# Kernel optimization log

Measured on AMD Instinct MI355X. Metric: run time of the kernel, lower is better.

Reference implementation:

```python
import jax, jax.numpy as jnp
import numpy as np

NUM_HEADS = 4   # num_heads init kwarg
KERNEL = 7      # kernel_size init kwarg
EPS = 1e-5      # nn.LayerNorm default eps


def setup_inputs() -> dict:
    key = jax.random.key(0)
    ks = jax.random.split(key, 6)
    C, depth = 128, 2
    x = jax.random.normal(ks[0], (2, C, 64, 64), jnp.float32)
    qkv_w = jax.random.normal(ks[1], (depth, 3 * C, C), jnp.float32) * 0.05
    qkv_b = jnp.zeros((depth, 3 * C), jnp.float32)
    rpb = jax.random.normal(ks[2], (depth, NUM_HEADS, 2 * KERNEL - 1, 2 * KERNEL - 1), jnp.float32) * 0.02
    proj_w = jax.random.normal(ks[3], (depth, C, C), jnp.float32) * 0.05
    proj_b = jnp.zeros((depth, C), jnp.float32)
    ln_g = jnp.ones((C,), jnp.float32)
    ln_b = jnp.zeros((C,), jnp.float32)
    return dict(x=x, qkv_w=qkv_w, qkv_b=qkv_b, rpb=rpb,
                proj_w=proj_w, proj_b=proj_b, ln_g=ln_g, ln_b=ln_b)


def _na2d(x, w_qkv, b_qkv, rpb, w_p, b_p):
    """NATTEN-style 2D neighborhood attention. x: (B,H,W,C)."""
    B, H, W, C = x.shape
    h, k = NUM_HEADS, KERNEL
    d = C // h
    qkv = (x @ w_qkv.T + b_qkv).reshape(B, H, W, 3, h, d)
    q = qkv[..., 0, :, :] * (d ** -0.5)   # (B,H,W,h,d)
    kk = qkv[..., 1, :, :]
    v = qkv[..., 2, :, :]
    # edge-clamped window starts: each query sees exactly k x k neighbors
    si = jnp.clip(jnp.arange(H) - k // 2, 0, H - k)
    sj = jnp.clip(jnp.arange(W) - k // 2, 0, W - k)
    idx_i = si[:, None] + jnp.arange(k)   # (H,k) absolute row indices
    idx_j = sj[:, None] + jnp.arange(k)   # (W,k) absolute col indices

    def win(t):  # (B,H,W,h,d) -> (B,H,W,k,k,h,d)
        t = t[:, idx_i]          # (B,H,k,W,h,d)
        t = t[:, :, :, idx_j]    # (B,H,k,W,k,h,d)
        return jnp.transpose(t, (0, 1, 3, 2, 4, 5, 6))

    kw = win(kk)
    vw = win(v)
    attn = jnp.einsum('bijhd,bijpqhd->bijhpq', q, kw)  # (B,H,W,h,k,k)
    # relative position bias: index = (neighbor_abs - query) + (k-1)
    bi = jnp.arange(k)[None, :] + (k - 1) - (jnp.arange(H) - si)[:, None]  # (H,k)
    bj = jnp.arange(k)[None, :] + (k - 1) - (jnp.arange(W) - sj)[:, None]  # (W,k)
    bias = rpb[:, bi[:, None, :, None], bj[None, :, None, :]]  # (h,H,W,k,k)
    attn = attn + jnp.transpose(bias, (1, 2, 0, 3, 4))[None]
    attn = jax.nn.softmax(attn.reshape(B, H, W, h, k * k), axis=-1).reshape(B, H, W, h, k, k)
    out = jnp.einsum('bijhpq,bijpqhd->bijhd', attn, vw).reshape(B, H, W, C)
    return out @ w_p.T + b_p


def reference(x, qkv_w, qkv_b, rpb, proj_w, proj_b, ln_g, ln_b):
    y = jnp.transpose(x, (0, 2, 3, 1))  # NCHW -> NHWC
    for l in range(qkv_w.shape[0]):     # depth=2 stacked NA layers
        y = _na2d(y, qkv_w[l], qkv_b[l], rpb[l], proj_w[l], proj_b[l])
    mu = y.mean(-1, keepdims=True)
    var = y.var(-1, keepdims=True)
    y = (y - mu) / jnp.sqrt(var + EPS) * ln_g + ln_b
    return jnp.transpose(y, (0, 3, 1, 2))  # NHWC -> NCHW
```

## Files before the change

### kernel.cpp

```cpp
#include <hip/hip_runtime.h>
#include <hip/hip_bf16.h>
#include <math.h>

#define PIX 8192
typedef __hip_bfloat16 bf16;
typedef __attribute__((ext_vector_type(8))) short short8;
typedef __attribute__((ext_vector_type(4))) float f32x4;

__device__ inline float bflo(unsigned u) { return __uint_as_float(u << 16); }
__device__ inline float bfhi(unsigned u) { return __uint_as_float(u & 0xffff0000u); }
__device__ inline unsigned short f2b(float f) {
  __hip_bfloat16 h = __float2bfloat16(f);
  return *reinterpret_cast<unsigned short*>(&h);
}
__device__ inline unsigned pack2(float a, float b) {
  return (unsigned)f2b(a) | ((unsigned)f2b(b) << 16);
}

__global__ __launch_bounds__(256) void prep(const float* __restrict__ x,
                                            const float* __restrict__ qw,
                                            const float* __restrict__ pw,
                                            unsigned short* __restrict__ y,
                                            unsigned short* __restrict__ wq,
                                            unsigned short* __restrict__ wp) {
  int tid = threadIdx.x;
  if (blockIdx.x >= 128) {
    int idx = (blockIdx.x - 128) * 256 + tid;
    if (idx < 98304) wq[idx] = f2b(qw[idx]);
    if (idx < 32768) wp[idx] = f2b(pw[idx]);
    return;
  }
  __shared__ float tile[64][129];
  int blk = blockIdx.x;
  int b = blk >> 6, i = blk & 63;
  const float* xbase = x + (size_t)b * 128 * 4096 + (size_t)i * 64;
  for (int idx = tid; idx < 8192; idx += 256) {
    int c = idx >> 6, j = idx & 63;
    tile[j][c] = xbase[(size_t)c * 4096 + j];
  }
  __syncthreads();
  unsigned short* yrow = y + (size_t)blk * 64 * 128;
  for (int idx = tid; idx < 8192; idx += 256) {
    int j = idx >> 7, c = idx & 127;
    yrow[idx] = f2b(tile[j][c]);
  }
}

__global__ __launch_bounds__(256) void gemm_mfma(const unsigned short* __restrict__ A,
                                                 const unsigned short* __restrict__ W,
                                                 const float* __restrict__ bias,
                                                 unsigned short* __restrict__ Cmat,
                                                 int N) {
  int m0 = blockIdx.x * 64, n0 = blockIdx.y * 64;
  int tid = threadIdx.x;
  int w = tid >> 6, lane = tid & 63;
  int quad = lane >> 4, l16 = lane & 15;

  const short8* ap =
      (const short8*)(A + (size_t)(m0 + w * 16 + l16) * 128 + quad * 8);
  short8 a[4];
#pragma unroll
  for (int kc = 0; kc < 4; ++kc) a[kc] = ap[kc * 4];

  f32x4 acc[4];
#pragma unroll
  for (int nt = 0; nt < 4; ++nt) {
    const short8* bp =
        (const short8*)(W + (size_t)(n0 + nt * 16 + l16) * 128 + quad * 8);
    f32x4 c = {0.f, 0.f, 0.f, 0.f};
#pragma unroll
    for (int kc = 0; kc < 4; ++kc)
      c = __builtin_amdgcn_mfma_f32_16x16x32_bf16(a[kc], bp[kc * 4], c, 0, 0, 0);
    acc[nt] = c;
  }

#pragma unroll
  for (int nt = 0; nt < 4; ++nt) {
    int col = n0 + nt * 16 + l16;
    float bv = bias[col];
#pragma unroll
    for (int r = 0; r < 4; ++r) {
      int m = m0 + w * 16 + quad * 4 + r;
      Cmat[(size_t)m * N + col] = f2b(acc[nt][r] + bv);
    }
  }
}

#define RSTRIDE 72
__global__ __launch_bounds__(256, 2) void na_attn(const unsigned short* __restrict__ qkvp,
                                                  const float* __restrict__ rpb,
                                                  unsigned short* __restrict__ out) {
  __shared__ __align__(16) unsigned short kbuf[140 * RSTRIDE];
  __shared__ __align__(16) unsigned short vbuf[140 * RSTRIDE];
  __shared__ float rb[338];
  __shared__ float sc[64][52];

  int ti = blockIdx.x >> 4, tj = blockIdx.x & 15;
  int hp = blockIdx.y;
  int bz = blockIdx.z;
  int tid = threadIdx.x;
  int bi0 = ti * 8 - 3, bj0 = tj * 4 - 3;

  for (int t = tid; t < 338; t += 256) rb[t] = rpb[hp * 338 + t];

  for (int t = tid; t < 2240; t += 256) {
    int row = t >> 4;
    int sub = t & 15;
    int isv = sub >> 3;
    int c = sub & 7;
    int ri = row / 10, rj = row - ri * 10;
    int gi = bi0 + ri, gj = bj0 + rj;
    uint4 val = make_uint4(0, 0, 0, 0);
    if ((unsigned)gi < 64u && (unsigned)gj < 64u) {
      int pixn = (bz * 64 + gi) * 64 + gj;
      val = *(const uint4*)(qkvp + (size_t)pixn * 384 + 128 + isv * 128 +
                            hp * 64 + c * 8);
    }
    *(uint4*)((isv ? vbuf : kbuf) + row * RSTRIDE + c * 8) = val;
  }
  __syncthreads();

  int r = tid & 3;
  int hl = (tid >> 2) & 1;
  int px = tid >> 3;
  int ph = px * 2 + hl;
  int pi = px >> 2, pj = px & 3;
  int i = ti * 8 + pi, j = tj * 4 + pj;
  int si = min(max(i - 3, 0), 57), sj = min(max(j - 3, 0), 57);
  int li = si - bi0, lj = sj - bj0;
  int oi = i - si, oj = j - sj;
  int H = hp * 2 + hl;
  int pix = (bz * 64 + i) * 64 + j;

  const float scale = 0.17677669529663687f;
  float q[8];
  {
    uint4 t = *(const uint4*)(qkvp + (size_t)pix * 384 + H * 32 + r * 8);
    q[0] = bflo(t.x) * scale;  q[1] = bfhi(t.x) * scale;
    q[2] = bflo(t.y) * scale;  q[3] = bfhi(t.y) * scale;
    q[4] = bflo(t.z) * scale;  q[5] = bfhi(t.z) * scale;
    q[6] = bflo(t.w) * scale;  q[7] = bfhi(t.w) * scale;
  }

  const unsigned short* kh = kbuf + hl * 32 + r * 8;
  const unsigned short* vh = vbuf + hl * 32 + r * 8;
  const float* rbh = rb + hl * 169;

#pragma unroll
  for (int p = 0; p < 7; ++p) {
#pragma unroll
    for (int qq = 0; qq < 7; ++qq) {
      int n = (li + p) * 10 + (lj + qq);
      uint4 t = *(const uint4*)(kh + n * RSTRIDE);
      float dot = q[0] * bflo(t.x) + q[1] * bfhi(t.x)
                + q[2] * bflo(t.y) + q[3] * bfhi(t.y)
                + q[4] * bflo(t.z) + q[5] * bfhi(t.z)
                + q[6] * bflo(t.w) + q[7] * bfhi(t.w);
      dot += __shfl_xor(dot, 1);
      dot += __shfl_xor(dot, 2);
      if (r == 0) sc[ph][p * 7 + qq] = dot + rbh[(p + 6 - oi) * 13 + (qq + 6 - oj)];
    }
  }
  __syncthreads();

  float m = -INFINITY;
#pragma unroll
  for (int n = 0; n < 49; ++n) m = fmaxf(m, sc[ph][n]);

  float sum = 0.f;
  float acc[8] = {0.f, 0.f, 0.f, 0.f, 0.f, 0.f, 0.f, 0.f};
#pragma unroll
  for (int p = 0; p < 7; ++p) {
#pragma unroll
    for (int qq = 0; qq < 7; ++qq) {
      float e = __expf(sc[ph][p * 7 + qq] - m);
      sum += e;
      int n = (li + p) * 10 + (lj + qq);
      uint4 t = *(const uint4*)(vh + n * RSTRIDE);
      acc[0] += e * bflo(t.x);  acc[1] += e * bfhi(t.x);
      acc[2] += e * bflo(t.y);  acc[3] += e * bfhi(t.y);
      acc[4] += e * bflo(t.z);  acc[5] += e * bfhi(t.z);
      acc[6] += e * bflo(t.w);  acc[7] += e * bfhi(t.w);
    }
  }
  float inv = 1.f / sum;
  uint4 t;
  t.x = pack2(acc[0] * inv, acc[1] * inv);
  t.y = pack2(acc[2] * inv, acc[3] * inv);
  t.z = pack2(acc[4] * inv, acc[5] * inv);
  t.w = pack2(acc[6] * inv, acc[7] * inv);
  *(uint4*)(out + (size_t)pix * 128 + H * 32 + r * 8) = t;
}

__global__ __launch_bounds__(256) void ln_out(const unsigned short* __restrict__ y,
                                              const float* __restrict__ g,
                                              const float* __restrict__ bta,
                                              float* __restrict__ out) {
  __shared__ float tile[64][129];
  __shared__ float mean_s[64], rstd_s[64];
  int blk = blockIdx.x;
  int b = blk >> 6, i = blk & 63;
  int tid = threadIdx.x;
  const unsigned short* yrow = y + (size_t)blk * 64 * 128;
  for (int idx = tid; idx < 8192; idx += 256) {
    int j = idx >> 7, c = idx & 127;
    tile[j][c] = __uint_as_float((unsigned)yrow[idx] << 16);
  }
  __syncthreads();
  int jj = tid >> 2, qtr = tid & 3;
  float sum = 0.f, sumsq = 0.f;
#pragma unroll
  for (int cc = 0; cc < 32; ++cc) {
    float v = tile[jj][qtr * 32 + cc];
    sum += v; sumsq += v * v;
  }
  sum += __shfl_xor(sum, 1);  sum += __shfl_xor(sum, 2);
  sumsq += __shfl_xor(sumsq, 1);  sumsq += __shfl_xor(sumsq, 2);
  if (qtr == 0) {
    float mu = sum * (1.f / 128.f);
    mean_s[jj] = mu;
    rstd_s[jj] = rsqrtf(sumsq * (1.f / 128.f) - mu * mu + 1e-5f);
  }
  __syncthreads();
  int c0 = tid >> 6;
  int j = tid & 63;
  for (int c = c0; c < 128; c += 4) {
    float v = (tile[j][c] - mean_s[j]) * rstd_s[j] * g[c] + bta[c];
    out[(((size_t)b * 128 + c) * 64 + i) * 64 + j] = v;
  }
}

extern "C" void kernel_launch(void* const* d_in, const int* in_sizes, int n_in,
                              void* d_out, int out_size, void* d_ws, size_t ws_size,
                              hipStream_t stream) {
  (void)in_sizes; (void)n_in; (void)out_size; (void)ws_size;
  const float* x   = (const float*)d_in[0];
  const float* qw  = (const float*)d_in[1];
  const float* qb  = (const float*)d_in[2];
  const float* rpb = (const float*)d_in[3];
  const float* pw  = (const float*)d_in[4];
  const float* pb  = (const float*)d_in[5];
  const float* lg  = (const float*)d_in[6];
  const float* lb  = (const float*)d_in[7];

  unsigned short* y    = (unsigned short*)d_ws;
  unsigned short* qkv  = y + (size_t)PIX * 128;
  unsigned short* wq   = qkv + (size_t)PIX * 384;
  unsigned short* wp   = wq + 98304;
  unsigned short* attn = (unsigned short*)d_out;
  float* out = (float*)d_out;

  prep<<<512, 256, 0, stream>>>(x, qw, pw, y, wq, wp);
  for (int l = 0; l < 2; ++l) {
    gemm_mfma<<<dim3(128, 6), 256, 0, stream>>>(y, wq + l * 49152, qb + l * 384, qkv, 384);
    na_attn<<<dim3(128, 2, 2), 256, 0, stream>>>(qkv, rpb + l * 676, attn);
    gemm_mfma<<<dim3(128, 2), 256, 0, stream>>>(attn, wp + l * 16384, pb + l * 128, y, 128);
  }
  ln_out<<<128, 256, 0, stream>>>(y, lg, lb, out);
}
```

Measured before the change: 146.6 us.

## Fuse layer-0 projection with layer-1 QKV GEMM and final projection with LayerNorm

Replaces the per-layer launch loop with a fixed sequence in which the layer-0 output projection and the layer-1 QKV projection run in one kernel, with the intermediate activations kept in shared memory. The final output projection is fused into the LayerNorm/transpose kernel. This removes two kernel launches and the global round-trip of the projected activations. In exchange, the fused kernels use only 128 blocks, which gives less parallelism than the separate GEMM grids. They also read weights directly from global memory without tiling.

Result: no change. 148.7 us (+1.4%).

```diff
diff --git a/kernel.cpp b/kernel.cpp
--- a/kernel.cpp
+++ b/kernel.cpp
@@ -192,21 +192,102 @@
   *(uint4*)(out + (size_t)pix * 128 + H * 32 + r * 8) = t;
 }
 
-__global__ __launch_bounds__(256) void ln_out(const unsigned short* __restrict__ y,
-                                              const float* __restrict__ g,
-                                              const float* __restrict__ bta,
-                                              float* __restrict__ out) {
+#define PSTRIDE 136
+__global__ __launch_bounds__(256) void projqkv(const unsigned short* __restrict__ attnp,
+                                               const unsigned short* __restrict__ wp0,
+                                               const float* __restrict__ pb0,
+                                               const unsigned short* __restrict__ wq1,
+                                               const float* __restrict__ qb1,
+                                               unsigned short* __restrict__ qkvout) {
+  __shared__ __align__(16) unsigned short po[64 * PSTRIDE];
+  int m0 = blockIdx.x * 64;
+  int tid = threadIdx.x;
+  int w = tid >> 6, lane = tid & 63;
+  int quad = lane >> 4, l16 = lane & 15;
+
+  {
+    const short8* ap =
+        (const short8*)(attnp + (size_t)(m0 + w * 16 + l16) * 128 + quad * 8);
+    short8 a[4];
+#pragma unroll
+    for (int kc = 0; kc < 4; ++kc) a[kc] = ap[kc * 4];
+#pragma unroll
+    for (int nt = 0; nt < 8; ++nt) {
+      const short8* bp =
+          (const short8*)(wp0 + (size_t)(nt * 16 + l16) * 128 + quad * 8);
+      f32x4 c = {0.f, 0.f, 0.f, 0.f};
+#pragma unroll
+      for (int kc = 0; kc < 4; ++kc)
+        c = __builtin_amdgcn_mfma_f32_16x16x32_bf16(a[kc], bp[kc * 4], c, 0, 0, 0);
+      float bv = pb0[nt * 16 + l16];
+#pragma unroll
+      for (int r2 = 0; r2 < 4; ++r2)
+        po[(w * 16 + quad * 4 + r2) * PSTRIDE + nt * 16 + l16] = f2b(c[r2] + bv);
+    }
+  }
+  __syncthreads();
+
+  {
+    short8 a[4];
+#pragma unroll
+    for (int kc = 0; kc < 4; ++kc)
+      a[kc] = *(const short8*)(po + (w * 16 + l16) * PSTRIDE + kc * 32 + quad * 8);
+#pragma unroll
+    for (int nt = 0; nt < 24; ++nt) {
+      const short8* bp =
+          (const short8*)(wq1 + (size_t)(nt * 16 + l16) * 128 + quad * 8);
+      f32x4 c = {0.f, 0.f, 0.f, 0.f};
+#pragma unroll
+      for (int kc = 0; kc < 4; ++kc)
+        c = __builtin_amdgcn_mfma_f32_16x16x32_bf16(a[kc], bp[kc * 4], c, 0, 0, 0);
+      int col = nt * 16 + l16;
+      float bv = qb1[col];
+#pragma unroll
+      for (int r2 = 0; r2 < 4; ++r2) {
+        int m = m0 + w * 16 + quad * 4 + r2;
+        qkvout[(size_t)m * 384 + col] = f2b(c[r2] + bv);
+      }
+    }
+  }
+}
+
+__global__ __launch_bounds__(256) void proj_ln(const unsigned short* __restrict__ attnp,
+                                               const unsigned short* __restrict__ wp1,
+                                               const float* __restrict__ pb1,
+                                               const float* __restrict__ g,
+                                               const float* __restrict__ bta,
+                                               float* __restrict__ out) {
   __shared__ float tile[64][129];
   __shared__ float mean_s[64], rstd_s[64];
   int blk = blockIdx.x;
   int b = blk >> 6, i = blk & 63;
-  int tid = threadIdx.x;
-  const unsigned short* yrow = y + (size_t)blk * 64 * 128;
-  for (int idx = tid; idx < 8192; idx += 256) {
-    int j = idx >> 7, c = idx & 127;
-    tile[j][c] = __uint_as_float((unsigned)yrow[idx] << 16);
-  }
-  __syncthreads();
+  int m0 = blk * 64;
+  int tid = threadIdx.x;
+  int w = tid >> 6, lane = tid & 63;
+  int quad = lane >> 4, l16 = lane & 15;
+
+  {
+    const short8* ap =
+        (const short8*)(attnp + (size_t)(m0 + w * 16 + l16) * 128 + quad * 8);
+    short8 a[4];
+#pragma unroll
+    for (int kc = 0; kc < 4; ++kc) a[kc] = ap[kc * 4];
+#pragma unroll
+    for (int nt = 0; nt < 8; ++nt) {
+      const short8* bp =
+          (const short8*)(wp1 + (size_t)(nt * 16 + l16) * 128 + quad * 8);
+      f32x4 c = {0.f, 0.f, 0.f, 0.f};
+#pragma unroll
+      for (int kc = 0; kc < 4; ++kc)
+        c = __builtin_amdgcn_mfma_f32_16x16x32_bf16(a[kc], bp[kc * 4], c, 0, 0, 0);
+      float bv = pb1[nt * 16 + l16];
+#pragma unroll
+      for (int r2 = 0; r2 < 4; ++r2)
+        tile[w * 16 + quad * 4 + r2][nt * 16 + l16] = c[r2] + bv;
+    }
+  }
+  __syncthreads();
+
   int jj = tid >> 2, qtr = tid & 3;
   float sum = 0.f, sumsq = 0.f;
 #pragma unroll
@@ -222,6 +303,7 @@
     rstd_s[jj] = rsqrtf(sumsq * (1.f / 128.f) - mu * mu + 1e-5f);
   }
   __syncthreads();
+
   int c0 = tid >> 6;
   int j = tid & 63;
   for (int c = c0; c < 128; c += 4) {
@@ -243,18 +325,16 @@
   const float* lg  = (const float*)d_in[6];
   const float* lb  = (const float*)d_in[7];
 
-  unsigned short* y    = (unsigned short*)d_ws;
-  unsigned short* qkv  = y + (size_t)PIX * 128;
+  unsigned short* ya   = (unsigned short*)d_ws;
+  unsigned short* qkv  = ya + (size_t)PIX * 128;
   unsigned short* wq   = qkv + (size_t)PIX * 384;
   unsigned short* wp   = wq + 98304;
-  unsigned short* attn = (unsigned short*)d_out;
   float* out = (float*)d_out;
 
-  prep<<<512, 256, 0, stream>>>(x, qw, pw, y, wq, wp);
-  for (int l = 0; l < 2; ++l) {
-    gemm_mfma<<<dim3(128, 6), 256, 0, stream>>>(y, wq + l * 49152, qb + l * 384, qkv, 384);
-    na_attn<<<dim3(128, 2, 2), 256, 0, stream>>>(qkv, rpb + l * 676, attn);
-    gemm_mfma<<<dim3(128, 2), 256, 0, stream>>>(attn, wp + l * 16384, pb + l * 128, y, 128);
-  }
-  ln_out<<<128, 256, 0, stream>>>(y, lg, lb, out);
-}
+  prep<<<512, 256, 0, stream>>>(x, qw, pw, ya, wq, wp);
+  gemm_mfma<<<dim3(128, 6), 256, 0, stream>>>(ya, wq, qb, qkv, 384);
+  na_attn<<<dim3(128, 2, 2), 256, 0, stream>>>(qkv, rpb, ya);
+  projqkv<<<128, 256, 0, stream>>>(ya, wp, pb, wq + 49152, qb + 384, qkv);
+  na_attn<<<dim3(128, 2, 2), 256, 0, stream>>>(qkv, rpb + 676, ya);
+  proj_ln<<<128, 256, 0, stream>>>(ya, wp + 16384, pb + 128, lg, lb, out);
+}
```
